# Optimization experiments

Hardware: AMD Instinct MI355X
Metric: run time of the kernel (lower is better)

The kernel has to match this reference:

```python
import jax, jax.numpy as jnp
import numpy as np

# ---- model dims (match init_kwargs) ----
B, L, D_MODEL = 2, 4096, 1024
EXPAND = 2
D_INNER = EXPAND * D_MODEL          # 2048
D_STATE = 128
D_CONV = 4
HEADDIM = 64
NHEADS = D_INNER // HEADDIM         # 32
NGROUPS = 1
CHUNK = 256
CONV_DIM = D_INNER + 2 * NGROUPS * D_STATE   # 2304
D_IN = 2 * D_INNER + 2 * NGROUPS * D_STATE + NHEADS  # 4384
EPS = 1e-5
DT_MIN, DT_MAX, DT_FLOOR = 0.001, 0.1, 1e-4
DT_LIMIT = (0.0, 100.0)
CONV_INIT = 0.5


def setup_inputs() -> dict:
    key = jax.random.key(0)
    ks = jax.random.split(key, 6)
    zxbcdt = jax.random.normal(ks[0], (B, L, D_IN), jnp.float32)
    conv_weight = jax.random.uniform(ks[1], (CONV_DIM, D_CONV), jnp.float32, -CONV_INIT, CONV_INIT)
    conv_b = jax.random.normal(ks[2], (CONV_DIM,), jnp.float32) * 0.01
    # dt_bias init: inverse softplus of dt sampled log-uniform in [dt_min, dt_max]
    dt = jnp.exp(jax.random.uniform(ks[3], (NHEADS,), jnp.float32) * (np.log(DT_MAX) - np.log(DT_MIN)) + np.log(DT_MIN))
    dt = jnp.clip(dt, DT_FLOOR, None)
    dt_bias = dt + jnp.log(-jnp.expm1(-dt))
    A_log = jnp.log(jax.random.uniform(ks[4], (NHEADS,), jnp.float32, 1.0, 16.0))
    Dparam = jnp.ones((NHEADS,), jnp.float32)
    norm_weight = jnp.ones((D_INNER,), jnp.float32)
    return dict(zxbcdt=zxbcdt, conv_weight=conv_weight, conv_b=conv_b,
                dt_bias=dt_bias, A_log=A_log, Dparam=Dparam, norm_weight=norm_weight)


def _segsum(x):
    """x: (..., T) -> (..., T, T), entry [i,j] = sum_{j<k<=i} x[k], -inf above diag."""
    T = x.shape[-1]
    xc = jnp.cumsum(x, axis=-1)
    seg = xc[..., :, None] - xc[..., None, :]
    mask = jnp.tril(jnp.ones((T, T), dtype=bool))
    return jnp.where(mask, seg, -jnp.inf)


def _ssd(x, a, Bm, Cm, chunk):
    """Chunked SSD (Mamba2). x:(b,l,h,p) already dt-scaled, a:(b,l,h)=dt*A,
    Bm/Cm:(b,l,h,n). Returns y:(b,l,h,p)."""
    b, l, h, p = x.shape
    n = Bm.shape[-1]
    c = l // chunk
    x = x.reshape(b, c, chunk, h, p)
    Bm = Bm.reshape(b, c, chunk, h, n)
    Cm = Cm.reshape(b, c, chunk, h, n)
    a = a.reshape(b, c, chunk, h).transpose(0, 3, 1, 2)  # (b,h,c,cl)
    a_cs = jnp.cumsum(a, axis=-1)                        # (b,h,c,cl)
    # 1) intra-chunk (diagonal blocks)
    Lmat = jnp.exp(_segsum(a))                           # (b,h,c,cl,cl)
    Y_diag = jnp.einsum('bclhn,bcshn,bhcls,bcshp->bclhp', Cm, Bm, Lmat, x)
    # 2) chunk final states
    decay_states = jnp.exp(a_cs[..., -1:] - a_cs)        # (b,h,c,cl)
    states = jnp.einsum('bclhn,bhcl,bclhp->bchpn', Bm, decay_states, x)
    states = jnp.concatenate([jnp.zeros_like(states[:, :1]), states], axis=1)  # (b,c+1,h,p,n)
    # 3) inter-chunk recurrence
    chunk_sum = jnp.pad(a_cs[..., -1], ((0, 0), (0, 0), (1, 0)))  # (b,h,c+1)
    decay_chunk = jnp.exp(_segsum(chunk_sum))            # (b,h,c+1,c+1)
    new_states = jnp.einsum('bhzc,bchpn->bzhpn', decay_chunk, states)
    prev_states = new_states[:, :-1]                     # (b,c,h,p,n)
    # 4) state -> output contribution
    Y_off = jnp.einsum('bclhn,bchpn,bhcl->bclhp', Cm, prev_states, jnp.exp(a_cs))
    return (Y_diag + Y_off).reshape(b, l, h, p)


def reference(zxbcdt, conv_weight, conv_b, dt_bias, A_log, Dparam, norm_weight):
    z, xBC, dt_raw = jnp.split(zxbcdt, [D_INNER, D_INNER + CONV_DIM], axis=-1)
    # depthwise causal conv1d (padding=d_conv-1, truncate to L) + SiLU
    xp = jnp.pad(xBC, ((0, 0), (D_CONV - 1, 0), (0, 0)))
    conv = conv_b
    for k in range(D_CONV):  # small fixed kernel width
        conv = conv + conv_weight[:, k] * xp[:, k:k + L, :]
    xBC = jax.nn.silu(conv)
    x, Bm, Cm = jnp.split(xBC, [D_INNER, D_INNER + NGROUPS * D_STATE], axis=-1)
    x = x.reshape(B, L, NHEADS, HEADDIM)
    hpg = NHEADS // NGROUPS
    Bm = jnp.repeat(Bm.reshape(B, L, NGROUPS, D_STATE), hpg, axis=2)  # (B,L,H,N)
    Cm = jnp.repeat(Cm.reshape(B, L, NGROUPS, D_STATE), hpg, axis=2)
    dt = jax.nn.softplus(dt_raw + dt_bias)               # (B,L,H)
    dt = jnp.clip(dt, DT_LIMIT[0], DT_LIMIT[1])
    A = -jnp.exp(A_log)                                  # (H,)
    y = _ssd(x * dt[..., None], dt * A, Bm, Cm, CHUNK)   # (B,L,H,P)
    y = y + x * Dparam[None, None, :, None]              # skip term D*x
    y = y.reshape(B, L, D_INNER)
    # gated RMSNorm (norm_before_gate=False): normalize(y * silu(z)) * w
    y = y * jax.nn.silu(z)
    y = y * jax.lax.rsqrt(jnp.mean(y * y, axis=-1, keepdims=True) + EPS) * norm_weight
    return y
```

## Files before the change

kernel.cpp:

```cpp
#include <hip/hip_runtime.h>
#include <hip/hip_bf16.h>

#define NB 2
#define LSEQ 4096
#define DIN 4384
#define DINNER 2048
#define DSTATE 128
#define CONVD 2304
#define HD 64
#define NH 32
#define CK 256
#define NCH 16

typedef __attribute__((ext_vector_type(8))) short bfrag;
typedef __attribute__((ext_vector_type(4))) float ffrag;

__device__ __forceinline__ float bf2f(unsigned short u){ return __uint_as_float(((unsigned int)u)<<16); }
__device__ __forceinline__ unsigned short f2bf(float f){
  unsigned int u = __float_as_uint(f);
  unsigned int r = (u + 0x7fffu + ((u>>16)&1u)) >> 16;
  return (unsigned short)r;
}
__device__ __forceinline__ unsigned int pk2(float a, float b){
  return (unsigned)f2bf(a) | ((unsigned)f2bf(b) << 16);
}
__device__ __forceinline__ float blo(unsigned int u){ return __uint_as_float(u<<16); }
__device__ __forceinline__ float bhi(unsigned int u){ return __uint_as_float(u & 0xffff0000u); }
__device__ __forceinline__ bfrag pack8(const float* f){
  bfrag r;
  #pragma unroll
  for (int i=0;i<8;i++) r[i] = (short)f2bf(f[i]);
  return r;
}

__global__ __launch_bounds__(256) void k_conv(const float* __restrict__ zx,
    const float* __restrict__ cw, const float* __restrict__ cb,
    unsigned short* __restrict__ xconv)
{
  int bid = blockIdx.x;
  int ct = bid % 9;
  int rt = bid / 9;
  int b = rt >> 6, lt = rt & 63;
  int t = threadIdx.x;
  int q = t & 63, lg = t >> 6;
  int c0 = ct*256 + q*4;
  const float* colp = zx + (size_t)b*LSEQ*DIN + DINNER + c0;
  float4 w0 = *(const float4*)&cw[(c0+0)*4];
  float4 w1 = *(const float4*)&cw[(c0+1)*4];
  float4 w2 = *(const float4*)&cw[(c0+2)*4];
  float4 w3 = *(const float4*)&cw[(c0+3)*4];
  float4 bias = *(const float4*)&cb[c0];
  int l0 = lt*64 + lg*16;
  float4 win0, win1, win2, win3;
  win0 = (l0-3 >= 0) ? *(const float4*)(colp + (size_t)(l0-3)*DIN) : make_float4(0,0,0,0);
  win1 = (l0-2 >= 0) ? *(const float4*)(colp + (size_t)(l0-2)*DIN) : make_float4(0,0,0,0);
  win2 = (l0-1 >= 0) ? *(const float4*)(colp + (size_t)(l0-1)*DIN) : make_float4(0,0,0,0);
  unsigned short* op = xconv + (size_t)(b*LSEQ)*CONVD + c0;
  #pragma unroll 4
  for (int i=0;i<16;i++){
    int l = l0 + i;
    win3 = *(const float4*)(colp + (size_t)l*DIN);
    float o0 = bias.x + w0.x*win0.x + w0.y*win1.x + w0.z*win2.x + w0.w*win3.x;
    float o1 = bias.y + w1.x*win0.y + w1.y*win1.y + w1.z*win2.y + w1.w*win3.y;
    float o2 = bias.z + w2.x*win0.z + w2.y*win1.z + w2.z*win2.z + w2.w*win3.z;
    float o3 = bias.w + w3.x*win0.w + w3.y*win1.w + w3.z*win2.w + w3.w*win3.w;
    o0 = o0 / (1.f + __expf(-o0));
    o1 = o1 / (1.f + __expf(-o1));
    o2 = o2 / (1.f + __expf(-o2));
    o3 = o3 / (1.f + __expf(-o3));
    uint2 pk; pk.x = pk2(o0,o1); pk.y = pk2(o2,o3);
    *(uint2*)&op[(size_t)l*CONVD] = pk;
    win0 = win1; win1 = win2; win2 = win3;
  }
}

__global__ __launch_bounds__(256) void k_dt(const float* __restrict__ zx,
    const float* __restrict__ dtb, float* __restrict__ dtv)
{
  int idx = blockIdx.x*256 + threadIdx.x;
  int l = idx & (LSEQ-1);
  int bh = idx >> 12;
  int h = bh & 31, b = bh >> 5;
  float x = zx[(size_t)(b*LSEQ + l)*DIN + DINNER + CONVD + h] + dtb[h];
  float sp = (x > 20.f) ? x : log1pf(__expf(x));
  dtv[idx] = fminf(sp, 100.f);
}

__global__ __launch_bounds__(256) void k_tr(const unsigned short* __restrict__ xconv,
    unsigned short* __restrict__ btg)
{
  __shared__ unsigned short sT[128][72];
  int bid = blockIdx.x;
  int b = bid >> 6, tile = bid & 63;
  int l0 = tile * 64;
  int t = threadIdx.x;
  #pragma unroll
  for (int k=0;k<32;k++){
    int idx = 256*k + t;
    int l = idx >> 7, n = idx & 127;
    sT[n][l] = xconv[(size_t)(b*LSEQ + l0 + l)*CONVD + DINNER + n];
  }
  __syncthreads();
  #pragma unroll
  for (int k=0;k<32;k++){
    int idx = 256*k + t;
    int n = idx >> 6, l = idx & 63;
    btg[(size_t)(b*DSTATE + n)*LSEQ + l0 + l] = sT[n][l];
  }
}

__global__ __launch_bounds__(256) void k_gmat(const unsigned short* __restrict__ xconv,
    unsigned short* __restrict__ G)
{
  int bid = blockIdx.x;
  int st = bid & 3, lt = (bid>>2)&3, c = (bid>>4)&15, b = bid>>8;
  if (st > lt) return;
  int t = threadIdx.x, lane = t & 63, wv = t >> 6;
  int cq = lane & 15, g = lane >> 4;
  const unsigned short* base = xconv + (size_t)(b*LSEQ + c*CK)*CONVD;
  ffrag acc[4];
  #pragma unroll
  for (int ss=0; ss<4; ++ss){ acc[ss][0]=0.f; acc[ss][1]=0.f; acc[ss][2]=0.f; acc[ss][3]=0.f; }
  #pragma unroll
  for (int ks=0; ks<4; ++ks){
    int nb = 32*ks + 8*g;
    int l = lt*64 + 16*wv + cq;
    bfrag afr = *(const bfrag*)(base + (size_t)l*CONVD + DINNER + DSTATE + nb);
    #pragma unroll
    for (int ss=0; ss<4; ++ss){
      int s = st*64 + 16*ss + cq;
      bfrag bfr = *(const bfrag*)(base + (size_t)s*CONVD + DINNER + nb);
      acc[ss] = __builtin_amdgcn_mfma_f32_16x16x32_bf16(afr, bfr, acc[ss], 0,0,0);
    }
  }
  unsigned short* gp = G + (size_t)(b*NCH + c)*CK*CK;
  #pragma unroll
  for (int ss=0; ss<4; ++ss)
    #pragma unroll
    for (int j=0; j<4; ++j){
      int l = lt*64 + 16*wv + 4*g + j, s = st*64 + 16*ss + cq;
      gp[(size_t)l*CK + s] = f2bf(acc[ss][j]);
    }
}

__global__ __launch_bounds__(256) void k_chunk(const unsigned short* __restrict__ xconv,
   const unsigned short* __restrict__ btg,
   const float* __restrict__ dtv, const float* __restrict__ alog,
   const unsigned short* __restrict__ G,
   unsigned short* __restrict__ states,
   float* __restrict__ acsg2, float* __restrict__ out)
{
  int bid = blockIdx.x;
  int h = bid & 31, c = (bid>>5)&15, b = bid>>9;
  int t = threadIdx.x, lane = t & 63, wv = t >> 6;
  int cq = lane & 15, g = lane >> 4;
  __shared__ float s_acs2[CK];
  __shared__ float s_w[CK];
  __shared__ float s_dt[CK];
  __shared__ unsigned short s_xsT[64][256];

  const float LOG2E = 1.44269504088896340736f;
  float dtl = dtv[(size_t)(b*NH + h)*LSEQ + c*CK + t];
  float a2 = dtl * (-__expf(alog[h])) * LOG2E;
  s_dt[t] = dtl;
  s_acs2[t] = a2;
  __syncthreads();
  #pragma unroll
  for (int off=1; off<256; off<<=1){
    float v = (t>=off) ? s_acs2[t-off] : 0.f;
    __syncthreads();
    s_acs2[t] += v;
    __syncthreads();
  }
  float a2last = s_acs2[CK-1];
  s_w[t] = exp2f(a2last - s_acs2[t]);
  acsg2[((size_t)(b*NCH + c)*NH + h)*CK + t] = s_acs2[t];
  {
    const unsigned short* xp = xconv + (size_t)(b*LSEQ + c*CK)*CONVD + h*HD;
    int p = t & 63;
    int lw = t >> 6;
    #pragma unroll 8
    for (int k=0;k<64;k++){
      int l = 4*k + lw;
      float x = bf2f(xp[(size_t)l*CONVD + p]);
      s_xsT[p][l ^ ((p&7)<<3)] = f2bf(x * s_dt[l]);
    }
  }
  __syncthreads();

  {
    ffrag acc[4][2];
    #pragma unroll
    for (int ps=0;ps<4;ps++)
      #pragma unroll
      for (int ns=0;ns<2;ns++){ acc[ps][ns][0]=0.f; acc[ps][ns][1]=0.f; acc[ps][ns][2]=0.f; acc[ps][ns][3]=0.f; }
    const unsigned short* btp = btg + (size_t)b*DSTATE*LSEQ + c*CK;
    #pragma unroll 2
    for (int ks=0; ks<8; ++ks){
      int lb = 32*ks + 8*g;
      float4 w0 = *(const float4*)&s_w[lb];
      float4 w1 = *(const float4*)&s_w[lb+4];
      bfrag bfr[2];
      #pragma unroll
      for (int ns=0; ns<2; ++ns){
        int n = 32*wv + 16*ns + cq;
        bfr[ns] = *(const bfrag*)(btp + (size_t)n*LSEQ + lb);
      }
      bfrag afr[4];
      #pragma unroll
      for (int ps=0; ps<4; ++ps){
        int p = 16*ps + cq;
        bfrag xv = *(const bfrag*)&s_xsT[p][lb ^ ((p&7)<<3)];
        float f[8];
        f[0]=bf2f((unsigned short)xv[0])*w0.x; f[1]=bf2f((unsigned short)xv[1])*w0.y;
        f[2]=bf2f((unsigned short)xv[2])*w0.z; f[3]=bf2f((unsigned short)xv[3])*w0.w;
        f[4]=bf2f((unsigned short)xv[4])*w1.x; f[5]=bf2f((unsigned short)xv[5])*w1.y;
        f[6]=bf2f((unsigned short)xv[6])*w1.z; f[7]=bf2f((unsigned short)xv[7])*w1.w;
        afr[ps] = pack8(f);
      }
      #pragma unroll
      for (int ps=0; ps<4; ++ps)
        #pragma unroll
        for (int ns=0; ns<2; ++ns)
          acc[ps][ns] = __builtin_amdgcn_mfma_f32_16x16x32_bf16(afr[ps], bfr[ns], acc[ps][ns], 0,0,0);
    }
    size_t sbase = ((size_t)((b*NCH + c)*NH + h))*HD*DSTATE;
    #pragma unroll
    for (int ps=0; ps<4; ++ps)
      #pragma unroll
      for (int ns=0; ns<2; ++ns)
        #pragma unroll
        for (int j=0; j<4; ++j){
          int p = 16*ps + 4*g + j, n = 32*wv + 16*ns + cq;
          states[sbase + (size_t)p*DSTATE + n] = f2bf(acc[ps][ns][j]);
        }
  }

  {
    ffrag acc[4][4];
    #pragma unroll
    for (int ls=0;ls<4;ls++)
      #pragma unroll
      for (int ps=0;ps<4;ps++){ acc[ls][ps][0]=0.f; acc[ls][ps][1]=0.f; acc[ls][ps][2]=0.f; acc[ls][ps][3]=0.f; }
    float a2l[4];
    #pragma unroll
    for (int ls=0; ls<4; ++ls) a2l[ls] = s_acs2[64*wv + 16*ls + cq];
    const unsigned short* gp = G + (size_t)(b*NCH + c)*CK*CK;
    int nks = 2*wv + 2;
    for (int ks=0; ks<nks; ++ks){
      int sb = 32*ks + 8*g;
      float4 e0 = *(const float4*)&s_acs2[sb];
      float4 e1 = *(const float4*)&s_acs2[sb+4];
      float a2s[8] = {e0.x,e0.y,e0.z,e0.w,e1.x,e1.y,e1.z,e1.w};
      bfrag bfr[4];
      #pragma unroll
      for (int ps=0; ps<4; ++ps){
        int p = 16*ps + cq;
        bfr[ps] = *(const bfrag*)&s_xsT[p][sb ^ ((p&7)<<3)];
      }
      bfrag afr[4];
      #pragma unroll
      for (int ls=0; ls<4; ++ls){
        int l = 64*wv + 16*ls + cq;
        bfrag gv = *(const bfrag*)(gp + (size_t)l*CK + sb);
        float f[8];
        #pragma unroll
        for (int i=0;i<8;i++){
          int s = sb + i;
          float cf = exp2f(a2l[ls] - a2s[i]);
          cf = (s <= l) ? cf : 0.f;
          f[i] = bf2f((unsigned short)gv[i]) * cf;
        }
        afr[ls] = pack8(f);
      }
      #pragma unroll
      for (int ls=0; ls<4; ++ls)
        #pragma unroll
        for (int ps=0; ps<4; ++ps)
          acc[ls][ps] = __builtin_amdgcn_mfma_f32_16x16x32_bf16(afr[ls], bfr[ps], acc[ls][ps], 0,0,0);
    }
    float* orow = out + (size_t)(b*LSEQ + c*CK)*DINNER + h*HD;
    #pragma unroll
    for (int ls=0; ls<4; ++ls)
      #pragma unroll
      for (int ps=0; ps<4; ++ps)
        #pragma unroll
        for (int j=0; j<4; ++j){
          int l = 64*wv + 16*ls + 4*g + j, p = 16*ps + cq;
          orow[(size_t)l*DINNER + p] = acc[ls][ps][j];
        }
  }
}

__global__ __launch_bounds__(256) void k_scan(unsigned short* __restrict__ states,
    const float* __restrict__ acsg2)
{
  int bid = blockIdx.x;
  int sub = bid & 7, h = (bid>>3) & 31, b = bid >> 8;
  int t = threadIdx.x;
  int e0 = sub*1024 + t*4;
  float c0=0.f, c1=0.f, c2=0.f, c3=0.f;
  for (int c=0;c<NCH;c++){
    float dec = exp2f(acsg2[((size_t)(b*NCH + c)*NH + h)*CK + (CK-1)]);
    size_t base = ((size_t)((b*NCH + c)*NH + h))*HD*DSTATE + e0;
    uint2 v = *(uint2*)&states[base];
    float u0 = blo(v.x), u1 = bhi(v.x), u2 = blo(v.y), u3 = bhi(v.y);
    uint2 w; w.x = pk2(c0,c1); w.y = pk2(c2,c3);
    *(uint2*)&states[base] = w;
    c0 = dec*c0 + u0; c1 = dec*c1 + u1; c2 = dec*c2 + u2; c3 = dec*c3 + u3;
  }
}

__global__ __launch_bounds__(256) void k_yoff(const unsigned short* __restrict__ xconv,
  const unsigned short* __restrict__ states, const float* __restrict__ acsg2,
  float* __restrict__ out)
{
  int bid = blockIdx.x;
  int h = bid & 31, c = (bid>>5)&15, b = bid>>9;
  int t = threadIdx.x, lane = t & 63, wv = t >> 6;
  int cq = lane & 15, g = lane >> 4;
  const float* ac = acsg2 + ((size_t)(b*NCH + c)*NH + h)*CK;
  const unsigned short* crow = xconv + (size_t)(b*LSEQ + c*CK)*CONVD + DINNER + DSTATE;
  const unsigned short* psb = states + ((size_t)((b*NCH + c)*NH + h))*HD*DSTATE;
  ffrag acc[4][4];
  #pragma unroll
  for (int ls=0;ls<4;ls++)
    #pragma unroll
    for (int pp=0;pp<4;pp++){ acc[ls][pp][0]=0.f; acc[ls][pp][1]=0.f; acc[ls][pp][2]=0.f; acc[ls][pp][3]=0.f; }
  #pragma unroll
  for (int ks=0; ks<4; ++ks){
    int nb = 32*ks + 8*g;
    bfrag bfr[4];
    #pragma unroll
    for (int pp=0; pp<4; ++pp)
      bfr[pp] = *(const bfrag*)(psb + (size_t)(16*pp + cq)*DSTATE + nb);
    bfrag afr[4];
    #pragma unroll
    for (int ls=0; ls<4; ++ls){
      int l = 64*wv + 16*ls + cq;
      afr[ls] = *(const bfrag*)(crow + (size_t)l*CONVD + nb);
    }
    #pragma unroll
    for (int ls=0; ls<4; ++ls)
      #pragma unroll
      for (int pp=0; pp<4; ++pp)
        acc[ls][pp] = __builtin_amdgcn_mfma_f32_16x16x32_bf16(afr[ls], bfr[pp], acc[ls][pp], 0,0,0);
  }
  float el[4][4];
  #pragma unroll
  for (int ls=0; ls<4; ++ls)
    #pragma unroll
    for (int j=0; j<4; ++j)
      el[ls][j] = exp2f(ac[64*wv + 16*ls + 4*g + j]);
  float* orow = out + (size_t)(b*LSEQ + c*CK)*DINNER + h*HD;
  #pragma unroll
  for (int ls=0; ls<4; ++ls)
    #pragma unroll
    for (int pp=0; pp<4; ++pp)
      #pragma unroll
      for (int j=0; j<4; ++j){
        int l = 64*wv + 16*ls + 4*g + j, p = 16*pp + cq;
        float* o = &orow[(size_t)l*DINNER + p];
        *o += el[ls][j] * acc[ls][pp][j];
      }
}

__global__ __launch_bounds__(256) void k_final(const float* __restrict__ zx,
  const unsigned short* __restrict__ xconv, const float* __restrict__ dpar,
  const float* __restrict__ nw, float* __restrict__ out)
{
  int row = blockIdx.x;
  int t = threadIdx.x;
  float* orow = out + (size_t)row*DINNER;
  const float* zrow = zx + (size_t)row*DIN;
  const unsigned short* xrow = xconv + (size_t)row*CONVD;
  float vals[8];
  float ss = 0.f;
  #pragma unroll
  for (int k=0;k<2;k++){
    int i4 = t + 256*k;
    float4 y4 = *(const float4*)&orow[4*i4];
    float yv[4] = {y4.x, y4.y, y4.z, y4.w};
    #pragma unroll
    for (int e=0;e<4;e++){
      int d = 4*i4 + e;
      int hh = d >> 6;
      float x = bf2f(xrow[d]);
      float y = yv[e] + x*dpar[hh];
      float z = zrow[d];
      y *= z / (1.f + __expf(-z));
      vals[4*k+e] = y;
      ss += y*y;
    }
  }
  #pragma unroll
  for (int off=1; off<64; off<<=1) ss += __shfl_xor(ss, off, 64);
  __shared__ float red[4];
  if ((t & 63) == 0) red[t>>6] = ss;
  __syncthreads();
  float tot = red[0]+red[1]+red[2]+red[3];
  float rms = rsqrtf(tot * (1.f/(float)DINNER) + 1e-5f);
  #pragma unroll
  for (int k=0;k<2;k++){
    int i4 = t + 256*k;
    float4 w4 = *(const float4*)&nw[4*i4];
    float4 o;
    o.x = vals[4*k+0]*rms*w4.x;
    o.y = vals[4*k+1]*rms*w4.y;
    o.z = vals[4*k+2]*rms*w4.z;
    o.w = vals[4*k+3]*rms*w4.w;
    *(float4*)&orow[4*i4] = o;
  }
}

extern "C" void kernel_launch(void* const* d_in, const int* in_sizes, int n_in,
                              void* d_out, int out_size, void* d_ws, size_t ws_size,
                              hipStream_t stream)
{
  const float* zx   = (const float*)d_in[0];
  const float* cw   = (const float*)d_in[1];
  const float* cb   = (const float*)d_in[2];
  const float* dtb  = (const float*)d_in[3];
  const float* alog = (const float*)d_in[4];
  const float* dpar = (const float*)d_in[5];
  const float* nw   = (const float*)d_in[6];
  float* out = (float*)d_out;
  char* ws = (char*)d_ws;

  unsigned short* xconv  = (unsigned short*)(ws);
  unsigned short* btg    = (unsigned short*)(ws + 37748736);
  float*          dtv    = (float*)(ws + 39845888);
  float*          acsg2  = (float*)(ws + 40894464);
  unsigned short* states = (unsigned short*)(ws + 41943040);
  unsigned short* G      = (unsigned short*)(ws + 58720256);

  hipLaunchKernelGGL(k_conv,  dim3(NB*64*9), dim3(256), 0, stream, zx, cw, cb, xconv);
  hipLaunchKernelGGL(k_dt,    dim3(1024),  dim3(256), 0, stream, zx, dtb, dtv);
  hipLaunchKernelGGL(k_tr,    dim3(NB*64), dim3(256), 0, stream, xconv, btg);
  hipLaunchKernelGGL(k_gmat,  dim3(NB*NCH*16), dim3(256), 0, stream, xconv, G);
  hipLaunchKernelGGL(k_chunk, dim3(NB*NCH*NH), dim3(256), 0, stream, xconv, btg, dtv, alog, G, states, acsg2, out);
  hipLaunchKernelGGL(k_scan,  dim3(NB*NH*8),  dim3(256), 0, stream, states, acsg2);
  hipLaunchKernelGGL(k_yoff,  dim3(NB*NCH*NH), dim3(256), 0, stream, xconv, states, acsg2, out);
  hipLaunchKernelGGL(k_final, dim3(NB*LSEQ), dim3(256), 0, stream, zx, xconv, dpar, nw, out);
}
```

Before: 383.0 us.

## Merge intra-chunk and inter-chunk output into one kernel with bf16 Y buffer

Moves the diagonal-block (G-masked) output computation out of the state kernel and fuses it with the off-diagonal state contribution in a new k_Y kernel. Both accumulate into a single register tile and write a bf16 intermediate, so the fp32 output is no longer written and then read-modify-written. k_final now reads the bf16 Y with vectorized loads. k_gmat launches only the lower-triangular tiles instead of launching and early-exiting the rest. In exchange, the x*dt transpose into shared memory is recomputed in both kernels, and Y is rounded to bf16 before the norm.

```diff
diff --git a/kernel.cpp b/kernel.cpp
--- a/kernel.cpp
+++ b/kernel.cpp
@@ -109,12 +109,16 @@
   }
 }
 
+__constant__ int g_lt[10] = {0,1,1,2,2,2,3,3,3,3};
+__constant__ int g_st[10] = {0,0,1,0,1,2,0,1,2,3};
 __global__ __launch_bounds__(256) void k_gmat(const unsigned short* __restrict__ xconv,
     unsigned short* __restrict__ G)
 {
   int bid = blockIdx.x;
-  int st = bid & 3, lt = (bid>>2)&3, c = (bid>>4)&15, b = bid>>8;
-  if (st > lt) return;
+  int pr = bid % 10;
+  int cc = bid / 10;
+  int c = cc & 15, b = cc >> 4;
+  int lt = g_lt[pr], st = g_st[pr];
   int t = threadIdx.x, lane = t & 63, wv = t >> 6;
   int cq = lane & 15, g = lane >> 4;
   const unsigned short* base = xconv + (size_t)(b*LSEQ + c*CK)*CONVD;
@@ -143,12 +147,11 @@
     }
 }
 
-__global__ __launch_bounds__(256) void k_chunk(const unsigned short* __restrict__ xconv,
+__global__ __launch_bounds__(256) void k_states(const unsigned short* __restrict__ xconv,
    const unsigned short* __restrict__ btg,
    const float* __restrict__ dtv, const float* __restrict__ alog,
-   const unsigned short* __restrict__ G,
    unsigned short* __restrict__ states,
-   float* __restrict__ acsg2, float* __restrict__ out)
+   float* __restrict__ acsg2)
 {
   int bid = blockIdx.x;
   int h = bid & 31, c = (bid>>5)&15, b = bid>>9;
@@ -188,108 +191,51 @@
   }
   __syncthreads();
 
-  {
-    ffrag acc[4][2];
-    #pragma unroll
-    for (int ps=0;ps<4;ps++)
-      #pragma unroll
-      for (int ns=0;ns<2;ns++){ acc[ps][ns][0]=0.f; acc[ps][ns][1]=0.f; acc[ps][ns][2]=0.f; acc[ps][ns][3]=0.f; }
-    const unsigned short* btp = btg + (size_t)b*DSTATE*LSEQ + c*CK;
-    #pragma unroll 2
-    for (int ks=0; ks<8; ++ks){
-      int lb = 32*ks + 8*g;
-      float4 w0 = *(const float4*)&s_w[lb];
-      float4 w1 = *(const float4*)&s_w[lb+4];
-      bfrag bfr[2];
-      #pragma unroll
-      for (int ns=0; ns<2; ++ns){
-        int n = 32*wv + 16*ns + cq;
-        bfr[ns] = *(const bfrag*)(btp + (size_t)n*LSEQ + lb);
+  ffrag acc[4][2];
+  #pragma unroll
+  for (int ps=0;ps<4;ps++)
+    #pragma unroll
+    for (int ns=0;ns<2;ns++){ acc[ps][ns][0]=0.f; acc[ps][ns][1]=0.f; acc[ps][ns][2]=0.f; acc[ps][ns][3]=0.f; }
+  const unsigned short* btp = btg + (size_t)b*DSTATE*LSEQ + c*CK;
+  #pragma unroll 2
+  for (int ks=0; ks<8; ++ks){
+    int lb = 32*ks + 8*g;
+    float4 w0 = *(const float4*)&s_w[lb];
+    float4 w1 = *(const float4*)&s_w[lb+4];
+    bfrag bfr[2];
+    #pragma unroll
+    for (int ns=0; ns<2; ++ns){
+      int n = 32*wv + 16*ns + cq;
+      bfr[ns] = *(const bfrag*)(btp + (size_t)n*LSEQ + lb);
+    }
+    bfrag afr[4];
+    #pragma unroll
+    for (int ps=0; ps<4; ++ps){
+      int p = 16*ps + cq;
+      bfrag xv = *(const bfrag*)&s_xsT[p][lb ^ ((p&7)<<3)];
+      float f[8];
+      f[0]=bf2f((unsigned short)xv[0])*w0.x; f[1]=bf2f((unsigned short)xv[1])*w0.y;
+      f[2]=bf2f((unsigned short)xv[2])*w0.z; f[3]=bf2f((unsigned short)xv[3])*w0.w;
+      f[4]=bf2f((unsigned short)xv[4])*w1.x; f[5]=bf2f((unsigned short)xv[5])*w1.y;
+      f[6]=bf2f((unsigned short)xv[6])*w1.z; f[7]=bf2f((unsigned short)xv[7])*w1.w;
+      afr[ps] = pack8(f);
+    }
+    #pragma unroll
+    for (int ps=0; ps<4; ++ps)
+      #pragma unroll
+      for (int ns=0; ns<2; ++ns)
+        acc[ps][ns] = __builtin_amdgcn_mfma_f32_16x16x32_bf16(afr[ps], bfr[ns], acc[ps][ns], 0,0,0);
+  }
+  size_t sbase = ((size_t)((b*NCH + c)*NH + h))*HD*DSTATE;
+  #pragma unroll
+  for (int ps=0; ps<4; ++ps)
+    #pragma unroll
+    for (int ns=0; ns<2; ++ns)
+      #pragma unroll
+      for (int j=0; j<4; ++j){
+        int p = 16*ps + 4*g + j, n = 32*wv + 16*ns + cq;
+        states[sbase + (size_t)p*DSTATE + n] = f2bf(acc[ps][ns][j]);
       }
-      bfrag afr[4];
-      #pragma unroll
-      for (int ps=0; ps<4; ++ps){
-        int p = 16*ps + cq;
-        bfrag xv = *(const bfrag*)&s_xsT[p][lb ^ ((p&7)<<3)];
-        float f[8];
-        f[0]=bf2f((unsigned short)xv[0])*w0.x; f[1]=bf2f((unsigned short)xv[1])*w0.y;
-        f[2]=bf2f((unsigned short)xv[2])*w0.z; f[3]=bf2f((unsigned short)xv[3])*w0.w;
-        f[4]=bf2f((unsigned short)xv[4])*w1.x; f[5]=bf2f((unsigned short)xv[5])*w1.y;
-        f[6]=bf2f((unsigned short)xv[6])*w1.z; f[7]=bf2f((unsigned short)xv[7])*w1.w;
-        afr[ps] = pack8(f);
-      }
-      #pragma unroll
-      for (int ps=0; ps<4; ++ps)
-        #pragma unroll
-        for (int ns=0; ns<2; ++ns)
-          acc[ps][ns] = __builtin_amdgcn_mfma_f32_16x16x32_bf16(afr[ps], bfr[ns], acc[ps][ns], 0,0,0);
-    }
-    size_t sbase = ((size_t)((b*NCH + c)*NH + h))*HD*DSTATE;
-    #pragma unroll
-    for (int ps=0; ps<4; ++ps)
-      #pragma unroll
-      for (int ns=0; ns<2; ++ns)
-        #pragma unroll
-        for (int j=0; j<4; ++j){
-          int p = 16*ps + 4*g + j, n = 32*wv + 16*ns + cq;
-          states[sbase + (size_t)p*DSTATE + n] = f2bf(acc[ps][ns][j]);
-        }
-  }
-
-  {
-    ffrag acc[4][4];
-    #pragma unroll
-    for (int ls=0;ls<4;ls++)
-      #pragma unroll
-      for (int ps=0;ps<4;ps++){ acc[ls][ps][0]=0.f; acc[ls][ps][1]=0.f; acc[ls][ps][2]=0.f; acc[ls][ps][3]=0.f; }
-    float a2l[4];
-    #pragma unroll
-    for (int ls=0; ls<4; ++ls) a2l[ls] = s_acs2[64*wv + 16*ls + cq];
-    const unsigned short* gp = G + (size_t)(b*NCH + c)*CK*CK;
-    int nks = 2*wv + 2;
-    for (int ks=0; ks<nks; ++ks){
-      int sb = 32*ks + 8*g;
-      float4 e0 = *(const float4*)&s_acs2[sb];
-      float4 e1 = *(const float4*)&s_acs2[sb+4];
-      float a2s[8] = {e0.x,e0.y,e0.z,e0.w,e1.x,e1.y,e1.z,e1.w};
-      bfrag bfr[4];
-      #pragma unroll
-      for (int ps=0; ps<4; ++ps){
-        int p = 16*ps + cq;
-        bfr[ps] = *(const bfrag*)&s_xsT[p][sb ^ ((p&7)<<3)];
-      }
-      bfrag afr[4];
-      #pragma unroll
-      for (int ls=0; ls<4; ++ls){
-        int l = 64*wv + 16*ls + cq;
-        bfrag gv = *(const bfrag*)(gp + (size_t)l*CK + sb);
-        float f[8];
-        #pragma unroll
-        for (int i=0;i<8;i++){
-          int s = sb + i;
-          float cf = exp2f(a2l[ls] - a2s[i]);
-          cf = (s <= l) ? cf : 0.f;
-          f[i] = bf2f((unsigned short)gv[i]) * cf;
-        }
-        afr[ls] = pack8(f);
-      }
-      #pragma unroll
-      for (int ls=0; ls<4; ++ls)
-        #pragma unroll
-        for (int ps=0; ps<4; ++ps)
-          acc[ls][ps] = __builtin_amdgcn_mfma_f32_16x16x32_bf16(afr[ls], bfr[ps], acc[ls][ps], 0,0,0);
-    }
-    float* orow = out + (size_t)(b*LSEQ + c*CK)*DINNER + h*HD;
-    #pragma unroll
-    for (int ls=0; ls<4; ++ls)
-      #pragma unroll
-      for (int ps=0; ps<4; ++ps)
-        #pragma unroll
-        for (int j=0; j<4; ++j){
-          int l = 64*wv + 16*ls + 4*g + j, p = 16*ps + cq;
-          orow[(size_t)l*DINNER + p] = acc[ls][ps][j];
-        }
-  }
 }
 
 __global__ __launch_bounds__(256) void k_scan(unsigned short* __restrict__ states,
@@ -311,87 +257,155 @@
   }
 }
 
-__global__ __launch_bounds__(256) void k_yoff(const unsigned short* __restrict__ xconv,
-  const unsigned short* __restrict__ states, const float* __restrict__ acsg2,
-  float* __restrict__ out)
+__global__ __launch_bounds__(256) void k_Y(const unsigned short* __restrict__ xconv,
+   const float* __restrict__ dtv,
+   const unsigned short* __restrict__ G,
+   const unsigned short* __restrict__ states,
+   const float* __restrict__ acsg2,
+   unsigned short* __restrict__ ybuf)
 {
   int bid = blockIdx.x;
   int h = bid & 31, c = (bid>>5)&15, b = bid>>9;
   int t = threadIdx.x, lane = t & 63, wv = t >> 6;
   int cq = lane & 15, g = lane >> 4;
-  const float* ac = acsg2 + ((size_t)(b*NCH + c)*NH + h)*CK;
-  const unsigned short* crow = xconv + (size_t)(b*LSEQ + c*CK)*CONVD + DINNER + DSTATE;
-  const unsigned short* psb = states + ((size_t)((b*NCH + c)*NH + h))*HD*DSTATE;
+  __shared__ float s_acs2[CK];
+  __shared__ float s_dt[CK];
+  __shared__ unsigned short s_xsT[64][256];
+
+  s_acs2[t] = acsg2[((size_t)(b*NCH + c)*NH + h)*CK + t];
+  s_dt[t] = dtv[(size_t)(b*NH + h)*LSEQ + c*CK + t];
+  __syncthreads();
+  {
+    const unsigned short* xp = xconv + (size_t)(b*LSEQ + c*CK)*CONVD + h*HD;
+    int p = t & 63;
+    int lw = t >> 6;
+    #pragma unroll 8
+    for (int k=0;k<64;k++){
+      int l = 4*k + lw;
+      float x = bf2f(xp[(size_t)l*CONVD + p]);
+      s_xsT[p][l ^ ((p&7)<<3)] = f2bf(x * s_dt[l]);
+    }
+  }
+  __syncthreads();
+
   ffrag acc[4][4];
   #pragma unroll
   for (int ls=0;ls<4;ls++)
     #pragma unroll
-    for (int pp=0;pp<4;pp++){ acc[ls][pp][0]=0.f; acc[ls][pp][1]=0.f; acc[ls][pp][2]=0.f; acc[ls][pp][3]=0.f; }
-  #pragma unroll
-  for (int ks=0; ks<4; ++ks){
-    int nb = 32*ks + 8*g;
+    for (int ps=0;ps<4;ps++){ acc[ls][ps][0]=0.f; acc[ls][ps][1]=0.f; acc[ls][ps][2]=0.f; acc[ls][ps][3]=0.f; }
+  float a2l[4];
+  #pragma unroll
+  for (int ls=0; ls<4; ++ls) a2l[ls] = s_acs2[64*wv + 16*ls + cq];
+
+  const unsigned short* gp = G + (size_t)(b*NCH + c)*CK*CK;
+  int nks = 2*wv + 2;
+  for (int ks=0; ks<nks; ++ks){
+    int sb = 32*ks + 8*g;
+    float4 e0 = *(const float4*)&s_acs2[sb];
+    float4 e1 = *(const float4*)&s_acs2[sb+4];
+    float a2s[8] = {e0.x,e0.y,e0.z,e0.w,e1.x,e1.y,e1.z,e1.w};
     bfrag bfr[4];
     #pragma unroll
-    for (int pp=0; pp<4; ++pp)
-      bfr[pp] = *(const bfrag*)(psb + (size_t)(16*pp + cq)*DSTATE + nb);
+    for (int ps=0; ps<4; ++ps){
+      int p = 16*ps + cq;
+      bfr[ps] = *(const bfrag*)&s_xsT[p][sb ^ ((p&7)<<3)];
+    }
     bfrag afr[4];
     #pragma unroll
     for (int ls=0; ls<4; ++ls){
       int l = 64*wv + 16*ls + cq;
-      afr[ls] = *(const bfrag*)(crow + (size_t)l*CONVD + nb);
+      bfrag gv = *(const bfrag*)(gp + (size_t)l*CK + sb);
+      float f[8];
+      #pragma unroll
+      for (int i=0;i<8;i++){
+        int s = sb + i;
+        float cf = exp2f(a2l[ls] - a2s[i]);
+        cf = (s <= l) ? cf : 0.f;
+        f[i] = bf2f((unsigned short)gv[i]) * cf;
+      }
+      afr[ls] = pack8(f);
     }
     #pragma unroll
     for (int ls=0; ls<4; ++ls)
       #pragma unroll
+      for (int ps=0; ps<4; ++ps)
+        acc[ls][ps] = __builtin_amdgcn_mfma_f32_16x16x32_bf16(afr[ls], bfr[ps], acc[ls][ps], 0,0,0);
+  }
+
+  {
+    float el[4];
+    #pragma unroll
+    for (int ls=0; ls<4; ++ls) el[ls] = exp2f(a2l[ls]);
+    const unsigned short* crow = xconv + (size_t)(b*LSEQ + c*CK)*CONVD + DINNER + DSTATE;
+    const unsigned short* psb = states + ((size_t)((b*NCH + c)*NH + h))*HD*DSTATE;
+    #pragma unroll
+    for (int ks=0; ks<4; ++ks){
+      int nb = 32*ks + 8*g;
+      bfrag bfr[4];
+      #pragma unroll
       for (int pp=0; pp<4; ++pp)
-        acc[ls][pp] = __builtin_amdgcn_mfma_f32_16x16x32_bf16(afr[ls], bfr[pp], acc[ls][pp], 0,0,0);
-  }
-  float el[4][4];
+        bfr[pp] = *(const bfrag*)(psb + (size_t)(16*pp + cq)*DSTATE + nb);
+      bfrag afr[4];
+      #pragma unroll
+      for (int ls=0; ls<4; ++ls){
+        int l = 64*wv + 16*ls + cq;
+        bfrag cv = *(const bfrag*)(crow + (size_t)l*CONVD + nb);
+        float f[8];
+        #pragma unroll
+        for (int i=0;i<8;i++) f[i] = bf2f((unsigned short)cv[i]) * el[ls];
+        afr[ls] = pack8(f);
+      }
+      #pragma unroll
+      for (int ls=0; ls<4; ++ls)
+        #pragma unroll
+        for (int pp=0; pp<4; ++pp)
+          acc[ls][pp] = __builtin_amdgcn_mfma_f32_16x16x32_bf16(afr[ls], bfr[pp], acc[ls][pp], 0,0,0);
+    }
+  }
+
+  unsigned short* yrow = ybuf + (size_t)(b*LSEQ + c*CK)*DINNER + h*HD;
   #pragma unroll
   for (int ls=0; ls<4; ++ls)
     #pragma unroll
-    for (int j=0; j<4; ++j)
-      el[ls][j] = exp2f(ac[64*wv + 16*ls + 4*g + j]);
-  float* orow = out + (size_t)(b*LSEQ + c*CK)*DINNER + h*HD;
-  #pragma unroll
-  for (int ls=0; ls<4; ++ls)
-    #pragma unroll
-    for (int pp=0; pp<4; ++pp)
+    for (int ps=0; ps<4; ++ps)
       #pragma unroll
       for (int j=0; j<4; ++j){
-        int l = 64*wv + 16*ls + 4*g + j, p = 16*pp + cq;
-        float* o = &orow[(size_t)l*DINNER + p];
-        *o += el[ls][j] * acc[ls][pp][j];
+        int l = 64*wv + 16*ls + 4*g + j, p = 16*ps + cq;
+        yrow[(size_t)l*DINNER + p] = f2bf(acc[ls][ps][j]);
       }
 }
 
 __global__ __launch_bounds__(256) void k_final(const float* __restrict__ zx,
-  const unsigned short* __restrict__ xconv, const float* __restrict__ dpar,
-  const float* __restrict__ nw, float* __restrict__ out)
+  const unsigned short* __restrict__ xconv, const unsigned short* __restrict__ ybuf,
+  const float* __restrict__ dpar, const float* __restrict__ nw,
+  float* __restrict__ out)
 {
   int row = blockIdx.x;
   int t = threadIdx.x;
-  float* orow = out + (size_t)row*DINNER;
+  int d0 = 8*t;
   const float* zrow = zx + (size_t)row*DIN;
   const unsigned short* xrow = xconv + (size_t)row*CONVD;
+  const unsigned short* yrow = ybuf + (size_t)row*DINNER;
   float vals[8];
   float ss = 0.f;
-  #pragma unroll
-  for (int k=0;k<2;k++){
-    int i4 = t + 256*k;
-    float4 y4 = *(const float4*)&orow[4*i4];
-    float yv[4] = {y4.x, y4.y, y4.z, y4.w};
-    #pragma unroll
-    for (int e=0;e<4;e++){
-      int d = 4*i4 + e;
-      int hh = d >> 6;
-      float x = bf2f(xrow[d]);
-      float y = yv[e] + x*dpar[hh];
-      float z = zrow[d];
-      y *= z / (1.f + __expf(-z));
-      vals[4*k+e] = y;
-      ss += y*y;
-    }
+  uint4 yv = *(const uint4*)&yrow[d0];
+  uint4 xv = *(const uint4*)&xrow[d0];
+  float4 z0 = *(const float4*)&zrow[d0];
+  float4 z1 = *(const float4*)&zrow[d0+4];
+  float dp = dpar[d0 >> 6];
+  float yf[8], xf[8];
+  yf[0]=blo(yv.x); yf[1]=bhi(yv.x); yf[2]=blo(yv.y); yf[3]=bhi(yv.y);
+  yf[4]=blo(yv.z); yf[5]=bhi(yv.z); yf[6]=blo(yv.w); yf[7]=bhi(yv.w);
+  xf[0]=blo(xv.x); xf[1]=bhi(xv.x); xf[2]=blo(xv.y); xf[3]=bhi(xv.y);
+  xf[4]=blo(xv.z); xf[5]=bhi(xv.z); xf[6]=blo(xv.w); xf[7]=bhi(xv.w);
+  float zf[8] = {z0.x,z0.y,z0.z,z0.w,z1.x,z1.y,z1.z,z1.w};
+  #pragma unroll
+  for (int e=0;e<8;e++){
+    float y = yf[e] + xf[e]*dp;
+    float z = zf[e];
+    y *= z / (1.f + __expf(-z));
+    vals[e] = y;
+    ss += y*y;
   }
   #pragma unroll
   for (int off=1; off<64; off<<=1) ss += __shfl_xor(ss, off, 64);
@@ -400,17 +414,16 @@
   __syncthreads();
   float tot = red[0]+red[1]+red[2]+red[3];
   float rms = rsqrtf(tot * (1.f/(float)DINNER) + 1e-5f);
-  #pragma unroll
-  for (int k=0;k<2;k++){
-    int i4 = t + 256*k;
-    float4 w4 = *(const float4*)&nw[4*i4];
-    float4 o;
-    o.x = vals[4*k+0]*rms*w4.x;
-    o.y = vals[4*k+1]*rms*w4.y;
-    o.z = vals[4*k+2]*rms*w4.z;
-    o.w = vals[4*k+3]*rms*w4.w;
-    *(float4*)&orow[4*i4] = o;
-  }
+  float* orow = out + (size_t)row*DINNER;
+  float4 w0 = *(const float4*)&nw[d0];
+  float4 w1 = *(const float4*)&nw[d0+4];
+  float4 o0, o1;
+  o0.x = vals[0]*rms*w0.x; o0.y = vals[1]*rms*w0.y;
+  o0.z = vals[2]*rms*w0.z; o0.w = vals[3]*rms*w0.w;
+  o1.x = vals[4]*rms*w1.x; o1.y = vals[5]*rms*w1.y;
+  o1.z = vals[6]*rms*w1.z; o1.w = vals[7]*rms*w1.w;
+  *(float4*)&orow[d0] = o0;
+  *(float4*)&orow[d0+4] = o1;
 }
 
 extern "C" void kernel_launch(void* const* d_in, const int* in_sizes, int n_in,
@@ -433,13 +446,14 @@
   float*          acsg2  = (float*)(ws + 40894464);
   unsigned short* states = (unsigned short*)(ws + 41943040);
   unsigned short* G      = (unsigned short*)(ws + 58720256);
-
-  hipLaunchKernelGGL(k_conv,  dim3(NB*64*9), dim3(256), 0, stream, zx, cw, cb, xconv);
-  hipLaunchKernelGGL(k_dt,    dim3(1024),  dim3(256), 0, stream, zx, dtb, dtv);
-  hipLaunchKernelGGL(k_tr,    dim3(NB*64), dim3(256), 0, stream, xconv, btg);
-  hipLaunchKernelGGL(k_gmat,  dim3(NB*NCH*16), dim3(256), 0, stream, xconv, G);
-  hipLaunchKernelGGL(k_chunk, dim3(NB*NCH*NH), dim3(256), 0, stream, xconv, btg, dtv, alog, G, states, acsg2, out);
-  hipLaunchKernelGGL(k_scan,  dim3(NB*NH*8),  dim3(256), 0, stream, states, acsg2);
-  hipLaunchKernelGGL(k_yoff,  dim3(NB*NCH*NH), dim3(256), 0, stream, xconv, states, acsg2, out);
-  hipLaunchKernelGGL(k_final, dim3(NB*LSEQ), dim3(256), 0, stream, zx, xconv, dpar, nw, out);
-}
+  unsigned short* ybuf   = (unsigned short*)(ws + 62914560);
+
+  hipLaunchKernelGGL(k_conv,   dim3(NB*64*9), dim3(256), 0, stream, zx, cw, cb, xconv);
+  hipLaunchKernelGGL(k_dt,     dim3(1024),  dim3(256), 0, stream, zx, dtb, dtv);
+  hipLaunchKernelGGL(k_tr,     dim3(NB*64), dim3(256), 0, stream, xconv, btg);
+  hipLaunchKernelGGL(k_gmat,   dim3(NB*NCH*10), dim3(256), 0, stream, xconv, G);
+  hipLaunchKernelGGL(k_states, dim3(NB*NCH*NH), dim3(256), 0, stream, xconv, btg, dtv, alog, states, acsg2);
+  hipLaunchKernelGGL(k_scan,   dim3(NB*NH*8),  dim3(256), 0, stream, states, acsg2);
+  hipLaunchKernelGGL(k_Y,      dim3(NB*NCH*NH), dim3(256), 0, stream, xconv, dtv, G, states, acsg2, ybuf);
+  hipLaunchKernelGGL(k_final,  dim3(NB*LSEQ), dim3(256), 0, stream, zx, xconv, ybuf, dpar, nw, out);
+}
```

Result: faster. 342.9 us (-10.5%).
